# Optimization experiments

Hardware: AMD Instinct MI355X
Metric: run time of the kernel (lower is better)

## Reference

```python
import jax, jax.numpy as jnp
import numpy as np

B, S = 256, 800
N1, N2 = 20000, 60000
NR = N1 + N2
E1, E2 = 60000, 180000
E1G, E2G = 15000, 45000
E1L, E2L = 15000, 45000
NSMT = 600
LAYER_FACTOR = 1e-2
NUM_ACTIVE_LAYERS = 2.0
EPS = 1e-30


def setup_inputs() -> dict:
    key = jax.random.key(0)
    ks = jax.random.split(key, 40)
    u = lambda i, sh: jax.random.uniform(ks[i], sh, jnp.float32)
    ri = lambda i, sh, lo, hi: jax.random.randint(ks[i], sh, lo, hi, dtype=jnp.int32)
    return {
        "t_in": u(0, (B,)),
        "y_in": u(1, (B, S)) * 1e-2,
        "den_gas": 1.0 + 1e4 * u(2, (B, 1)),
        "T_gas": 10.0 + 290.0 * u(3, (B, 1)),
        "alpha": u(4, (NR,)),
        "beta": u(5, (NR,)) * 2.0 - 1.0,
        "gamma": u(6, (NR,)) * 50.0,
        "k1": ri(7, (E1,), 0, N1), "r1": ri(8, (E1,), 0, S), "p1": ri(9, (E1,), 0, S), "s1": ri(10, (E1,), 0, 2),
        "k2": ri(11, (E2,), N1, NR), "ra2": ri(12, (E2,), 0, S), "rb2": ri(13, (E2,), 0, S), "p2": ri(14, (E2,), 0, S), "s2": ri(15, (E2,), 0, 2),
        "k1g": ri(16, (E1G,), 0, N1), "r1g": ri(17, (E1G,), 0, S), "p1g": ri(18, (E1G,), 0, S), "s1g": ri(19, (E1G,), 0, 2),
        "k2g": ri(20, (E2G,), N1, NR), "ra2g": ri(21, (E2G,), 0, S), "rb2g": ri(22, (E2G,), 0, S), "p2g": ri(23, (E2G,), 0, S), "s2g": ri(24, (E2G,), 0, 2),
        "k1l": ri(25, (E1L,), 0, N1), "r1l": ri(26, (E1L,), 0, S), "p1l": ri(27, (E1L,), 0, S), "s1l": ri(28, (E1L,), 0, 2),
        "k2l": ri(29, (E2L,), N1, NR), "ra2l": ri(30, (E2L,), 0, S), "rb2l": ri(31, (E2L,), 0, S), "p2l": ri(32, (E2L,), 0, S), "s2l": ri(33, (E2L,), 0, 2),
        "inds_surf": jnp.arange(200, 500, dtype=jnp.int32),
        "inds_mant": jnp.arange(500, 800, dtype=jnp.int32),
        "inds_smt_s2m": jnp.arange(0, NSMT, dtype=jnp.int32),
        "inds_smt_m2s": jnp.arange(NSMT, 2 * NSMT, dtype=jnp.int32),
    }


def _sgn(s):
    return 2.0 * s.astype(jnp.float32) - 1.0


def _asm1(y, coeffs, k, r, p, s):
    # 1st-order: gather rate coeff + reactant, scatter signed rate into product
    rates = coeffs[:, k] * y[:, r] * _sgn(s)  # [B, E]
    return jnp.zeros((y.shape[0], S), y.dtype).at[:, p].add(rates)


def _asm2(y, coeffs, den, k, ra, rb, p, s):
    # 2nd-order: coeff * y_a * y_b * den_gas, scatter into product
    rates = coeffs[:, k] * y[:, ra] * y[:, rb] * den * _sgn(s)  # [B, E]
    return jnp.zeros((y.shape[0], S), y.dtype).at[:, p].add(rates)


def _forward(t_in, y_in, den_gas, T_gas, alpha, beta, gamma,
             k1, r1, p1, s1, k2, ra2, rb2, p2, s2,
             k1g, r1g, p1g, s1g, k2g, ra2g, rb2g, p2g, s2g,
             k1l, r1l, p1l, s1l, k2l, ra2l, rb2l, p2l, s2l,
             inds_surf, inds_mant, inds_smt_s2m, inds_smt_m2s):
    den = den_gas  # [B,1] density normalization for 2nd-order reactions
    T = T_gas      # [B,1]
    # modified-Arrhenius rate coefficients (rmod.assign_rate_coeffs), [B, NR]
    coeffs = alpha * (T / 300.0) ** beta * jnp.exp(-gamma / T)
    y_surf = y_in[:, inds_surf].sum(-1, keepdims=True)
    y_mant = y_in[:, inds_mant].sum(-1, keepdims=True)
    n_layer_surf = LAYER_FACTOR * y_surf
    n_layer_mant = LAYER_FACTOR * y_mant
    decay = jnp.minimum(NUM_ACTIVE_LAYERS / jnp.maximum(n_layer_surf + n_layer_mant, EPS), 1.0)
    # surface gain/loss assemblers, restricted to surface species then summed
    dy_gain = (_asm1(y_in, coeffs, k1g, r1g, p1g, s1g)
               + _asm2(y_in, coeffs, den, k2g, ra2g, rb2g, p2g, s2g))[:, inds_surf]
    dy_surf_gain = dy_gain.sum(-1, keepdims=True)
    dy_loss = (_asm1(y_in, coeffs, k1l, r1l, p1l, s1l)
               + _asm2(y_in, coeffs, den, k2l, ra2l, rb2l, p2l, s2l))[:, inds_surf]
    dy_surf_loss = -dy_loss.sum(-1, keepdims=True)
    # rmod_smt: surface<->mantle swap rate coefficients scatter-set into coeffs
    Bn = y_in.shape[0]
    k_s2m = jnp.broadcast_to(dy_surf_gain / jnp.maximum(y_surf, EPS), (Bn, NSMT))
    k_m2s = jnp.broadcast_to(-dy_surf_loss / jnp.maximum(y_mant, EPS) * decay, (Bn, NSMT))
    coeffs = coeffs.at[:, inds_smt_s2m].set(k_s2m)
    coeffs = coeffs.at[:, inds_smt_m2s].set(k_m2s)
    # final RHS: asm_1st + asm_2nd over all reactions
    return (_asm1(y_in, coeffs, k1, r1, p1, s1)
            + _asm2(y_in, coeffs, den, k2, ra2, rb2, p2, s2))


def reference(t_in, y_in, den_gas, T_gas, alpha, beta, gamma,
              k1, r1, p1, s1, k2, ra2, rb2, p2, s2,
              k1g, r1g, p1g, s1g, k2g, ra2g, rb2g, p2g, s2g,
              k1l, r1l, p1l, s1l, k2l, ra2l, rb2l, p2l, s2l,
              inds_surf, inds_mant, inds_smt_s2m, inds_smt_m2s):
    return _forward(t_in, y_in, den_gas, T_gas, alpha, beta, gamma,
                    k1, r1, p1, s1, k2, ra2, rb2, p2, s2,
                    k1g, r1g, p1g, s1g, k2g, ra2g, rb2g, p2g, s2g,
                    k1l, r1l, p1l, s1l, k2l, ra2l, rb2l, p2l, s2l,
                    inds_surf, inds_mant, inds_smt_s2m, inds_smt_m2s)
```

## Files before the change

### kernel.cpp

```cpp
#include <hip/hip_runtime.h>


constexpr int B_    = 256;
constexpr int S_    = 800;
constexpr int E1_   = 60000;
constexpr int E2_   = 180000;
constexpr int ET_   = E1_ + E2_;
constexpr int EGL_  = 120000;
constexpr int NSMT_ = 600;
constexpr float LOG2E_ = 1.4426950408889634f;
constexpr float EPS_   = 1e-30f;
constexpr int PAD   = 16;
constexpr int CAPP  = 512;
constexpr int CAP_  = 32768;
constexpr int NBGL_ = 1024;
constexpr int NSL_  = 8;
constexpr int NB_T  = 200;
constexpr int NB_P  = (EGL_ + 255) / 256;
constexpr int NB_R  = (ET_ + 255) / 256;
constexpr int IB_ONE = 800, IB_KS = 801, IB_KM = 802, WROWS = 804;

#if defined(__has_builtin)
#if __has_builtin(__builtin_amdgcn_exp2f)
#define FAST_EXP2(x) __builtin_amdgcn_exp2f(x)
#endif
#endif
#ifndef FAST_EXP2
#define FAST_EXP2(x) exp2f(x)
#endif

__global__ __launch_bounds__(256) void prep_kernel(
    const float* __restrict__ y, const float* __restrict__ den_gas,
    float* __restrict__ yT, float* __restrict__ wT,
    const float* __restrict__ alpha, const float* __restrict__ beta,
    const float* __restrict__ gam,
    const int* __restrict__ k1g, const int* __restrict__ r1g,
    const int* __restrict__ p1g, const int* __restrict__ s1g,
    const int* __restrict__ k2g, const int* __restrict__ ra2g,
    const int* __restrict__ rb2g, const int* __restrict__ p2g,
    const int* __restrict__ s2g,
    const int* __restrict__ k1l, const int* __restrict__ r1l,
    const int* __restrict__ p1l, const int* __restrict__ s1l,
    const int* __restrict__ k2l, const int* __restrict__ ra2l,
    const int* __restrict__ rb2l, const int* __restrict__ p2l,
    const int* __restrict__ s2l,
    int* __restrict__ glcnt, float4* __restrict__ glG, float4* __restrict__ glL)
{
    __shared__ float tile[32][33];
    __shared__ int cntW[2][4];
    __shared__ int baseS[2];

    const int blk = blockIdx.x;
    const int tid = threadIdx.x;

    if (blk < NB_T) {
        const int bi = blk;
        const int sb = bi % 25, bb = bi / 25;
        const int tx = tid & 31, ty = tid >> 5;
        const int s0 = sb * 32, b0 = bb * 32;
        #pragma unroll
        for (int j = 0; j < 4; ++j) {
            int bl = ty + 8 * j;
            tile[bl][tx] = y[(b0 + bl) * S_ + s0 + tx];
        }
        __syncthreads();
        const float d = den_gas[b0 + tx];
        #pragma unroll
        for (int j = 0; j < 4; ++j) {
            int sl = ty + 8 * j;
            float v = tile[tx][sl];
            yT[(s0 + sl) * B_ + b0 + tx] = v;
            wT[(s0 + sl) * B_ + b0 + tx] = v * d;
        }
        if (bi == 0) wT[IB_ONE * B_ + tid] = 1.0f;
        return;
    }
    {
        const int lane = tid & 63, wid = tid >> 6;
        const int e = (blk - NB_T) * 256 + tid;

        int kk = 0, ia = 0, ib = 0, pp = -1, ss = 0, gl = 0;
        if (e < EGL_) {
            if (e < 15000)      { int i = e;         kk = k1g[i]; ia = r1g[i];  ib = IB_ONE;  pp = p1g[i]; ss = s1g[i]; gl = 0; }
            else if (e < 60000) { int i = e - 15000; kk = k2g[i]; ia = ra2g[i]; ib = rb2g[i]; pp = p2g[i]; ss = s2g[i]; gl = 0; }
            else if (e < 75000) { int i = e - 60000; kk = k1l[i]; ia = r1l[i];  ib = IB_ONE;  pp = p1l[i]; ss = s1l[i]; gl = 1; }
            else                { int i = e - 75000; kk = k2l[i]; ia = ra2l[i]; ib = rb2l[i]; pp = p2l[i]; ss = s2l[i]; gl = 1; }
        }
        const bool keep = (pp >= 200 && pp < 500);
        const bool kG = keep && (gl == 0);
        const bool kL = keep && (gl == 1);

        const unsigned long long mG = __ballot(kG);
        const unsigned long long mL = __ballot(kL);
        if (lane == 0) { cntW[0][wid] = __popcll(mG); cntW[1][wid] = __popcll(mL); }
        __syncthreads();
        if (tid < 2) {
            int s = 0;
            #pragma unroll
            for (int w = 0; w < 4; ++w) { int v = cntW[tid][w]; cntW[tid][w] = s; s += v; }
            baseS[tid] = s ? atomicAdd(&glcnt[tid], s) : 0;
        }
        __syncthreads();

        if (keep) {
            float a = alpha[kk], b = beta[kk], g = gam[kk];
            float a_s = ss ? a : -a;
            int bits = ia | (ib << 10);
            const unsigned long long lt = (1ull << lane) - 1ull;
            if (kG) {
                int slot = baseS[0] + cntW[0][wid] + __popcll(mG & lt);
                glG[slot] = make_float4(a_s, b, g, __int_as_float(bits));
            } else {
                int slot = baseS[1] + cntW[1][wid] + __popcll(mL & lt);
                glL[slot] = make_float4(a_s, b, g, __int_as_float(bits));
            }
        }
    }
}

__device__ __forceinline__ float edge_term(
    float4 q, int t, const float* __restrict__ yT, const float* __restrict__ wT,
    float lt2, float nivt)
{
    int bu = __builtin_amdgcn_readfirstlane(__float_as_int(q.w));
    int ia = bu & 1023, ib = (bu >> 10) & 1023;
    return q.x * FAST_EXP2(fmaf(q.y, lt2, q.z * nivt))
         * yT[ia * B_ + t] * wT[ib * B_ + t];
}

__global__ __launch_bounds__(256) void work_kernel(
    const float* __restrict__ alpha, const float* __restrict__ beta,
    const float* __restrict__ gam,
    const int* __restrict__ k1, const int* __restrict__ r1,
    const int* __restrict__ p1, const int* __restrict__ s1,
    const int* __restrict__ k2, const int* __restrict__ ra2,
    const int* __restrict__ rb2, const int* __restrict__ p2,
    const int* __restrict__ s2,
    int* __restrict__ rank, float4* __restrict__ bucket,
    const float* __restrict__ T_gas,
    const float* __restrict__ yT, const float* __restrict__ wT,
    const float4* __restrict__ glG, const float4* __restrict__ glL,
    const int* __restrict__ glcnt,
    float* __restrict__ part_sl)
{
    __shared__ float4 tG[CAP_ / NBGL_], tL[CAP_ / NBGL_];
    const int blk = blockIdx.x;
    const int tid = threadIdx.x;

    if (blk < NB_R) {
        int e = blk * 256 + tid;
        if (e >= ET_) return;
        int kk, ia, ib, pp, ss;
        if (e < E1_) {
            kk = k1[e]; ia = r1[e]; pp = p1[e]; ss = s1[e]; ib = IB_ONE;
        } else {
            int i = e - E1_;
            kk = k2[i]; ia = ra2[i]; ib = rb2[i]; pp = p2[i]; ss = s2[i];
        }
        float a = alpha[kk], b = beta[kk], g = gam[kk];
        if (e < E1_ && kk < 2 * NSMT_) {
            ib = (kk < NSMT_) ? IB_KS : IB_KM;
            a = 1.0f; b = 0.0f; g = 0.0f;
        }
        float a_s = ss ? a : -a;
        int bits = ia | (ib << 10);
        int slot = atomicAdd(&rank[pp * PAD], 1);
        bucket[pp * CAPP + slot] = make_float4(a_s, b, g, __int_as_float(bits));
        return;
    }
    {
        const int t = tid, c = blk - NB_R;
        const int nG = glcnt[0], nL = glcnt[1];
        const int cG = (nG + NBGL_ - 1) >> 10;
        const int cL = (nL + NBGL_ - 1) >> 10;
        const int g0 = c * cG, gn = min(nG, g0 + cG) - g0;
        const int l0 = c * cL, ln = min(nL, l0 + cL) - l0;
        for (int i = t; i < gn; i += 256) tG[i] = glG[g0 + i];
        for (int i = t; i < ln; i += 256) tL[i] = glL[l0 + i];
        __syncthreads();

        const float T    = T_gas[t];
        const float lt2  = log2f(T * (1.0f / 300.0f));
        const float nivt = -LOG2E_ / T;

        float gain = 0.f, loss = 0.f;
        #pragma unroll 4
        for (int i = 0; i < gn; ++i) gain += edge_term(tG[i], t, yT, wT, lt2, nivt);
        #pragma unroll 4
        for (int i = 0; i < ln; ++i) loss += edge_term(tL[i], t, yT, wT, lt2, nivt);

        float* sl = part_sl + (c & (NSL_ - 1)) * (2 * B_);
        atomicAdd(&sl[2 * t + 0], gain);
        atomicAdd(&sl[2 * t + 1], loss);
    }
}

__global__ __launch_bounds__(256) void ksm_kernel(
    const float* __restrict__ y, const float* __restrict__ part_sl,
    float* __restrict__ wT)
{
    const int lane = threadIdx.x & 63, wid = threadIdx.x >> 6;
    const int b = blockIdx.x * 4 + wid;
    float vs = 0.f, vm = 0.f;
    #pragma unroll
    for (int j = 0; j < 5; ++j) {
        int i = lane + 64 * j;
        if (i < 300) { vs += y[b * S_ + 200 + i]; vm += y[b * S_ + 500 + i]; }
    }
    #pragma unroll
    for (int o = 32; o > 0; o >>= 1) {
        vs += __shfl_down(vs, o, 64);
        vm += __shfl_down(vm, o, 64);
    }
    if (lane == 0) {
        float gain = 0.f, loss = 0.f;
        #pragma unroll
        for (int s = 0; s < NSL_; ++s) {
            gain += part_sl[s * (2 * B_) + 2 * b + 0];
            loss += part_sl[s * (2 * B_) + 2 * b + 1];
        }
        float nl = 1e-2f * (vs + vm);
        float decay = fminf(2.0f / fmaxf(nl, EPS_), 1.0f);
        wT[IB_KS * B_ + b] = gain / fmaxf(vs, EPS_);
        wT[IB_KM * B_ + b] = loss / fmaxf(vm, EPS_) * decay;
    }
}

__global__ __launch_bounds__(256) void final_kernel(
    const float* __restrict__ T_gas,
    const float* __restrict__ yT, const float* __restrict__ wT,
    const float4* __restrict__ bucket, const int* __restrict__ rank,
    float* __restrict__ outT)
{
    __shared__ float4 tile[CAPP / 2 + 8];
    const int t = threadIdx.x;
    const int p = blockIdx.x >> 1, h = blockIdx.x & 1;
    const int n  = rank[p * PAD];
    const int n0 = n >> 1;
    const int s0 = h ? n0 : 0;
    const int s1 = h ? n  : n0;
    const int cnt = s1 - s0;

    const float4* src = bucket + p * CAPP + s0;
    for (int i = t; i < cnt; i += 256) tile[i] = src[i];
    __syncthreads();

    const float T    = T_gas[t];
    const float lt2  = log2f(T * (1.0f / 300.0f));
    const float nivt = -LOG2E_ / T;

    float acc = 0.f;
    int i = 0;
    #pragma unroll 1
    for (; i + 8 <= cnt; i += 8) {
        float4 q0 = tile[i + 0], q1 = tile[i + 1];
        float4 q2 = tile[i + 2], q3 = tile[i + 3];
        float4 q4 = tile[i + 4], q5 = tile[i + 5];
        float4 q6 = tile[i + 6], q7 = tile[i + 7];
        int b0 = __builtin_amdgcn_readfirstlane(__float_as_int(q0.w));
        int b1 = __builtin_amdgcn_readfirstlane(__float_as_int(q1.w));
        int b2 = __builtin_amdgcn_readfirstlane(__float_as_int(q2.w));
        int b3 = __builtin_amdgcn_readfirstlane(__float_as_int(q3.w));
        int b4 = __builtin_amdgcn_readfirstlane(__float_as_int(q4.w));
        int b5 = __builtin_amdgcn_readfirstlane(__float_as_int(q5.w));
        int b6 = __builtin_amdgcn_readfirstlane(__float_as_int(q6.w));
        int b7 = __builtin_amdgcn_readfirstlane(__float_as_int(q7.w));
        float y0 = yT[(b0 & 1023) * B_ + t], w0 = wT[((b0 >> 10) & 1023) * B_ + t];
        float y1 = yT[(b1 & 1023) * B_ + t], w1 = wT[((b1 >> 10) & 1023) * B_ + t];
        float y2 = yT[(b2 & 1023) * B_ + t], w2 = wT[((b2 >> 10) & 1023) * B_ + t];
        float y3 = yT[(b3 & 1023) * B_ + t], w3 = wT[((b3 >> 10) & 1023) * B_ + t];
        float y4 = yT[(b4 & 1023) * B_ + t], w4 = wT[((b4 >> 10) & 1023) * B_ + t];
        float y5 = yT[(b5 & 1023) * B_ + t], w5 = wT[((b5 >> 10) & 1023) * B_ + t];
        float y6 = yT[(b6 & 1023) * B_ + t], w6 = wT[((b6 >> 10) & 1023) * B_ + t];
        float y7 = yT[(b7 & 1023) * B_ + t], w7 = wT[((b7 >> 10) & 1023) * B_ + t];
        float t0 = q0.x * FAST_EXP2(fmaf(q0.y, lt2, q0.z * nivt)) * y0 * w0;
        float t1 = q1.x * FAST_EXP2(fmaf(q1.y, lt2, q1.z * nivt)) * y1 * w1;
        float t2 = q2.x * FAST_EXP2(fmaf(q2.y, lt2, q2.z * nivt)) * y2 * w2;
        float t3 = q3.x * FAST_EXP2(fmaf(q3.y, lt2, q3.z * nivt)) * y3 * w3;
        float t4 = q4.x * FAST_EXP2(fmaf(q4.y, lt2, q4.z * nivt)) * y4 * w4;
        float t5 = q5.x * FAST_EXP2(fmaf(q5.y, lt2, q5.z * nivt)) * y5 * w5;
        float t6 = q6.x * FAST_EXP2(fmaf(q6.y, lt2, q6.z * nivt)) * y6 * w6;
        float t7 = q7.x * FAST_EXP2(fmaf(q7.y, lt2, q7.z * nivt)) * y7 * w7;
        acc += ((t0 + t1) + (t2 + t3)) + ((t4 + t5) + (t6 + t7));
    }
    for (; i < cnt; ++i) {
        float4 q = tile[i];
        int bu = __builtin_amdgcn_readfirstlane(__float_as_int(q.w));
        float yv = yT[(bu & 1023) * B_ + t], wv = wT[((bu >> 10) & 1023) * B_ + t];
        acc += q.x * FAST_EXP2(fmaf(q.y, lt2, q.z * nivt)) * yv * wv;
    }

    atomicAdd(&outT[p * B_ + t], acc);
}

__global__ __launch_bounds__(256) void transpose_out_kernel(
    const float* __restrict__ outT, float* __restrict__ out)
{
    __shared__ float tile[32][33];
    const int sb = blockIdx.x % 25, bb = blockIdx.x / 25;
    const int tx = threadIdx.x & 31, ty = threadIdx.x >> 5;
    const int s0 = sb * 32, b0 = bb * 32;

    #pragma unroll
    for (int j = 0; j < 4; ++j) {
        int sl = ty + 8 * j;
        tile[sl][tx] = outT[(s0 + sl) * B_ + b0 + tx];
    }
    __syncthreads();
    #pragma unroll
    for (int j = 0; j < 4; ++j) {
        int bl = ty + 8 * j;
        out[(b0 + bl) * S_ + s0 + tx] = tile[tx][bl];
    }
}

extern "C" void kernel_launch(void* const* d_in, const int* in_sizes, int n_in,
                              void* d_out, int out_size, void* d_ws, size_t ws_size,
                              hipStream_t stream) {
    const float* y       = (const float*)d_in[1];
    const float* den_gas = (const float*)d_in[2];
    const float* T_gas   = (const float*)d_in[3];
    const float* alpha   = (const float*)d_in[4];
    const float* beta    = (const float*)d_in[5];
    const float* gam     = (const float*)d_in[6];
    const int* k1  = (const int*)d_in[7];
    const int* r1  = (const int*)d_in[8];
    const int* p1  = (const int*)d_in[9];
    const int* s1  = (const int*)d_in[10];
    const int* k2  = (const int*)d_in[11];
    const int* ra2 = (const int*)d_in[12];
    const int* rb2 = (const int*)d_in[13];
    const int* p2  = (const int*)d_in[14];
    const int* s2  = (const int*)d_in[15];
    const int* k1g  = (const int*)d_in[16];
    const int* r1g  = (const int*)d_in[17];
    const int* p1g  = (const int*)d_in[18];
    const int* s1g  = (const int*)d_in[19];
    const int* k2g  = (const int*)d_in[20];
    const int* ra2g = (const int*)d_in[21];
    const int* rb2g = (const int*)d_in[22];
    const int* p2g  = (const int*)d_in[23];
    const int* s2g  = (const int*)d_in[24];
    const int* k1l  = (const int*)d_in[25];
    const int* r1l  = (const int*)d_in[26];
    const int* p1l  = (const int*)d_in[27];
    const int* s1l  = (const int*)d_in[28];
    const int* k2l  = (const int*)d_in[29];
    const int* ra2l = (const int*)d_in[30];
    const int* rb2l = (const int*)d_in[31];
    const int* p2l  = (const int*)d_in[32];
    const int* s2l  = (const int*)d_in[33];

    char* wsp = (char*)d_ws;
    size_t off = 0;
    float4* bucket = (float4*)(wsp + off); off += (size_t)S_ * CAPP * 16;
    float4* glG    = (float4*)(wsp + off); off += (size_t)CAP_ * 16;
    float4* glL    = (float4*)(wsp + off); off += (size_t)CAP_ * 16;
    float*  yT     = (float*)(wsp + off);  off += (size_t)S_ * B_ * 4;
    float*  wT     = (float*)(wsp + off);  off += (size_t)WROWS * B_ * 4;
    size_t zoff = off;
    float*  outT    = (float*)(wsp + off); off += (size_t)S_ * B_ * 4;
    int*    rank    = (int*)(wsp + off);   off += (size_t)S_ * PAD * 4;
    float*  part_sl = (float*)(wsp + off); off += (size_t)NSL_ * 2 * B_ * 4;
    int*    glcnt   = (int*)(wsp + off);   off += 64;
    size_t zbytes = off - zoff;

    float* out = (float*)d_out;

    hipMemsetAsync(wsp + zoff, 0, zbytes, stream);

    prep_kernel<<<NB_T + NB_P, 256, 0, stream>>>(
        y, den_gas, yT, wT,
        alpha, beta, gam,
        k1g, r1g, p1g, s1g, k2g, ra2g, rb2g, p2g, s2g,
        k1l, r1l, p1l, s1l, k2l, ra2l, rb2l, p2l, s2l,
        glcnt, glG, glL);

    work_kernel<<<NB_R + NBGL_, 256, 0, stream>>>(
        alpha, beta, gam, k1, r1, p1, s1, k2, ra2, rb2, p2, s2,
        rank, bucket,
        T_gas, yT, wT, glG, glL, glcnt, part_sl);

    ksm_kernel<<<64, 256, 0, stream>>>(y, part_sl, wT);

    final_kernel<<<2 * S_, 256, 0, stream>>>(T_gas, yT, wT, bucket, rank, outT);
    transpose_out_kernel<<<200, 256, 0, stream>>>(outT, out);
}
```

Measured before the change: 78.75 us.

## Fuse ksm and output transpose into final kernel, compute surface/mantle sums in prep

Surface and mantle row sums now come from the prep transpose blocks through LDS and global atomics. The swap coefficients are computed per thread inside the final kernel and substituted for the special wT rows. Each product row gets one block that writes the output directly without an atomic, which removes the ksm kernel, the outT buffer and the transpose kernel. The cost is halving the final grid to 800 blocks, adding per-edge selects, and writing output with a strided, uncoalesced pattern.

```diff
diff --git a/kernel.cpp b/kernel.cpp
--- a/kernel.cpp
+++ b/kernel.cpp
@@ -32,6 +32,7 @@
 __global__ __launch_bounds__(256) void prep_kernel(
     const float* __restrict__ y, const float* __restrict__ den_gas,
     float* __restrict__ yT, float* __restrict__ wT,
+    float* __restrict__ vsum, float* __restrict__ msum,
     const float* __restrict__ alpha, const float* __restrict__ beta,
     const float* __restrict__ gam,
     const int* __restrict__ k1g, const int* __restrict__ r1g,
@@ -47,6 +48,7 @@
     int* __restrict__ glcnt, float4* __restrict__ glG, float4* __restrict__ glL)
 {
     __shared__ float tile[32][33];
+    __shared__ float lds_vs[32], lds_vm[32];
     __shared__ int cntW[2][4];
     __shared__ int baseS[2];
 
@@ -58,6 +60,7 @@
         const int sb = bi % 25, bb = bi / 25;
         const int tx = tid & 31, ty = tid >> 5;
         const int s0 = sb * 32, b0 = bb * 32;
+        if (tid < 32) { lds_vs[tid] = 0.0f; lds_vm[tid] = 0.0f; }
         #pragma unroll
         for (int j = 0; j < 4; ++j) {
             int bl = ty + 8 * j;
@@ -65,12 +68,24 @@
         }
         __syncthreads();
         const float d = den_gas[b0 + tx];
+        float vsp = 0.0f, vmp = 0.0f;
         #pragma unroll
         for (int j = 0; j < 4; ++j) {
             int sl = ty + 8 * j;
+            int s  = s0 + sl;
             float v = tile[tx][sl];
             yT[(s0 + sl) * B_ + b0 + tx] = v;
             wT[(s0 + sl) * B_ + b0 + tx] = v * d;
+            if (s >= 200 && s < 500)      vsp += v;
+            else if (s >= 500)            vmp += v;
+        }
+        if (vsp != 0.0f) atomicAdd(&lds_vs[tx], vsp);
+        if (vmp != 0.0f) atomicAdd(&lds_vm[tx], vmp);
+        __syncthreads();
+        if (tid < 32) {
+            float a = lds_vs[tid], m = lds_vm[tid];
+            if (a != 0.0f) atomicAdd(&vsum[b0 + tid], a);
+            if (m != 0.0f) atomicAdd(&msum[b0 + tid], m);
         }
         if (bi == 0) wT[IB_ONE * B_ + tid] = 1.0f;
         return;
@@ -195,59 +210,38 @@
     }
 }
 
-__global__ __launch_bounds__(256) void ksm_kernel(
-    const float* __restrict__ y, const float* __restrict__ part_sl,
-    float* __restrict__ wT)
-{
-    const int lane = threadIdx.x & 63, wid = threadIdx.x >> 6;
-    const int b = blockIdx.x * 4 + wid;
-    float vs = 0.f, vm = 0.f;
-    #pragma unroll
-    for (int j = 0; j < 5; ++j) {
-        int i = lane + 64 * j;
-        if (i < 300) { vs += y[b * S_ + 200 + i]; vm += y[b * S_ + 500 + i]; }
-    }
-    #pragma unroll
-    for (int o = 32; o > 0; o >>= 1) {
-        vs += __shfl_down(vs, o, 64);
-        vm += __shfl_down(vm, o, 64);
-    }
-    if (lane == 0) {
-        float gain = 0.f, loss = 0.f;
-        #pragma unroll
-        for (int s = 0; s < NSL_; ++s) {
-            gain += part_sl[s * (2 * B_) + 2 * b + 0];
-            loss += part_sl[s * (2 * B_) + 2 * b + 1];
-        }
-        float nl = 1e-2f * (vs + vm);
-        float decay = fminf(2.0f / fmaxf(nl, EPS_), 1.0f);
-        wT[IB_KS * B_ + b] = gain / fmaxf(vs, EPS_);
-        wT[IB_KM * B_ + b] = loss / fmaxf(vm, EPS_) * decay;
-    }
-}
-
 __global__ __launch_bounds__(256) void final_kernel(
     const float* __restrict__ T_gas,
     const float* __restrict__ yT, const float* __restrict__ wT,
     const float4* __restrict__ bucket, const int* __restrict__ rank,
-    float* __restrict__ outT)
+    const float* __restrict__ part_sl,
+    const float* __restrict__ vsum, const float* __restrict__ msum,
+    float* __restrict__ out)
 {
-    __shared__ float4 tile[CAPP / 2 + 8];
+    __shared__ float4 tile[CAPP];
     const int t = threadIdx.x;
-    const int p = blockIdx.x >> 1, h = blockIdx.x & 1;
-    const int n  = rank[p * PAD];
-    const int n0 = n >> 1;
-    const int s0 = h ? n0 : 0;
-    const int s1 = h ? n  : n0;
-    const int cnt = s1 - s0;
-
-    const float4* src = bucket + p * CAPP + s0;
+    const int p = blockIdx.x;
+    const int cnt = rank[p * PAD];
+
+    const float4* src = bucket + p * CAPP;
     for (int i = t; i < cnt; i += 256) tile[i] = src[i];
-    __syncthreads();
+
+    float gain = 0.f, loss = 0.f;
+    #pragma unroll
+    for (int s = 0; s < NSL_; ++s) {
+        gain += part_sl[s * (2 * B_) + 2 * t + 0];
+        loss += part_sl[s * (2 * B_) + 2 * t + 1];
+    }
+    const float vs = vsum[t], vm = msum[t];
+    const float nl = 1e-2f * (vs + vm);
+    const float decay = fminf(2.0f / fmaxf(nl, EPS_), 1.0f);
+    const float ks = gain / fmaxf(vs, EPS_);
+    const float km = loss / fmaxf(vm, EPS_) * decay;
 
     const float T    = T_gas[t];
     const float lt2  = log2f(T * (1.0f / 300.0f));
     const float nivt = -LOG2E_ / T;
+    __syncthreads();
 
     float acc = 0.f;
     int i = 0;
@@ -265,14 +259,26 @@
         int b5 = __builtin_amdgcn_readfirstlane(__float_as_int(q5.w));
         int b6 = __builtin_amdgcn_readfirstlane(__float_as_int(q6.w));
         int b7 = __builtin_amdgcn_readfirstlane(__float_as_int(q7.w));
-        float y0 = yT[(b0 & 1023) * B_ + t], w0 = wT[((b0 >> 10) & 1023) * B_ + t];
-        float y1 = yT[(b1 & 1023) * B_ + t], w1 = wT[((b1 >> 10) & 1023) * B_ + t];
-        float y2 = yT[(b2 & 1023) * B_ + t], w2 = wT[((b2 >> 10) & 1023) * B_ + t];
-        float y3 = yT[(b3 & 1023) * B_ + t], w3 = wT[((b3 >> 10) & 1023) * B_ + t];
-        float y4 = yT[(b4 & 1023) * B_ + t], w4 = wT[((b4 >> 10) & 1023) * B_ + t];
-        float y5 = yT[(b5 & 1023) * B_ + t], w5 = wT[((b5 >> 10) & 1023) * B_ + t];
-        float y6 = yT[(b6 & 1023) * B_ + t], w6 = wT[((b6 >> 10) & 1023) * B_ + t];
-        float y7 = yT[(b7 & 1023) * B_ + t], w7 = wT[((b7 >> 10) & 1023) * B_ + t];
+        int i0 = (b0 >> 10) & 1023, i1 = (b1 >> 10) & 1023;
+        int i2 = (b2 >> 10) & 1023, i3 = (b3 >> 10) & 1023;
+        int i4 = (b4 >> 10) & 1023, i5 = (b5 >> 10) & 1023;
+        int i6 = (b6 >> 10) & 1023, i7 = (b7 >> 10) & 1023;
+        float y0 = yT[(b0 & 1023) * B_ + t], w0 = wT[i0 * B_ + t];
+        float y1 = yT[(b1 & 1023) * B_ + t], w1 = wT[i1 * B_ + t];
+        float y2 = yT[(b2 & 1023) * B_ + t], w2 = wT[i2 * B_ + t];
+        float y3 = yT[(b3 & 1023) * B_ + t], w3 = wT[i3 * B_ + t];
+        float y4 = yT[(b4 & 1023) * B_ + t], w4 = wT[i4 * B_ + t];
+        float y5 = yT[(b5 & 1023) * B_ + t], w5 = wT[i5 * B_ + t];
+        float y6 = yT[(b6 & 1023) * B_ + t], w6 = wT[i6 * B_ + t];
+        float y7 = yT[(b7 & 1023) * B_ + t], w7 = wT[i7 * B_ + t];
+        w0 = (i0 == IB_KS) ? ks : ((i0 == IB_KM) ? km : w0);
+        w1 = (i1 == IB_KS) ? ks : ((i1 == IB_KM) ? km : w1);
+        w2 = (i2 == IB_KS) ? ks : ((i2 == IB_KM) ? km : w2);
+        w3 = (i3 == IB_KS) ? ks : ((i3 == IB_KM) ? km : w3);
+        w4 = (i4 == IB_KS) ? ks : ((i4 == IB_KM) ? km : w4);
+        w5 = (i5 == IB_KS) ? ks : ((i5 == IB_KM) ? km : w5);
+        w6 = (i6 == IB_KS) ? ks : ((i6 == IB_KM) ? km : w6);
+        w7 = (i7 == IB_KS) ? ks : ((i7 == IB_KM) ? km : w7);
         float t0 = q0.x * FAST_EXP2(fmaf(q0.y, lt2, q0.z * nivt)) * y0 * w0;
         float t1 = q1.x * FAST_EXP2(fmaf(q1.y, lt2, q1.z * nivt)) * y1 * w1;
         float t2 = q2.x * FAST_EXP2(fmaf(q2.y, lt2, q2.z * nivt)) * y2 * w2;
@@ -286,32 +292,14 @@
     for (; i < cnt; ++i) {
         float4 q = tile[i];
         int bu = __builtin_amdgcn_readfirstlane(__float_as_int(q.w));
-        float yv = yT[(bu & 1023) * B_ + t], wv = wT[((bu >> 10) & 1023) * B_ + t];
+        int ibx = (bu >> 10) & 1023;
+        float yv = yT[(bu & 1023) * B_ + t];
+        float wv = wT[ibx * B_ + t];
+        wv = (ibx == IB_KS) ? ks : ((ibx == IB_KM) ? km : wv);
         acc += q.x * FAST_EXP2(fmaf(q.y, lt2, q.z * nivt)) * yv * wv;
     }
 
-    atomicAdd(&outT[p * B_ + t], acc);
-}
-
-__global__ __launch_bounds__(256) void transpose_out_kernel(
-    const float* __restrict__ outT, float* __restrict__ out)
-{
-    __shared__ float tile[32][33];
-    const int sb = blockIdx.x % 25, bb = blockIdx.x / 25;
-    const int tx = threadIdx.x & 31, ty = threadIdx.x >> 5;
-    const int s0 = sb * 32, b0 = bb * 32;
-
-    #pragma unroll
-    for (int j = 0; j < 4; ++j) {
-        int sl = ty + 8 * j;
-        tile[sl][tx] = outT[(s0 + sl) * B_ + b0 + tx];
-    }
-    __syncthreads();
-    #pragma unroll
-    for (int j = 0; j < 4; ++j) {
-        int bl = ty + 8 * j;
-        out[(b0 + bl) * S_ + s0 + tx] = tile[tx][bl];
-    }
+    out[t * S_ + p] = acc;
 }
 
 extern "C" void kernel_launch(void* const* d_in, const int* in_sizes, int n_in,
@@ -359,9 +347,10 @@
     float*  yT     = (float*)(wsp + off);  off += (size_t)S_ * B_ * 4;
     float*  wT     = (float*)(wsp + off);  off += (size_t)WROWS * B_ * 4;
     size_t zoff = off;
-    float*  outT    = (float*)(wsp + off); off += (size_t)S_ * B_ * 4;
     int*    rank    = (int*)(wsp + off);   off += (size_t)S_ * PAD * 4;
     float*  part_sl = (float*)(wsp + off); off += (size_t)NSL_ * 2 * B_ * 4;
+    float*  vsum    = (float*)(wsp + off); off += (size_t)B_ * 4;
+    float*  msum    = (float*)(wsp + off); off += (size_t)B_ * 4;
     int*    glcnt   = (int*)(wsp + off);   off += 64;
     size_t zbytes = off - zoff;
 
@@ -370,7 +359,7 @@
     hipMemsetAsync(wsp + zoff, 0, zbytes, stream);
 
     prep_kernel<<<NB_T + NB_P, 256, 0, stream>>>(
-        y, den_gas, yT, wT,
+        y, den_gas, yT, wT, vsum, msum,
         alpha, beta, gam,
         k1g, r1g, p1g, s1g, k2g, ra2g, rb2g, p2g, s2g,
         k1l, r1l, p1l, s1l, k2l, ra2l, rb2l, p2l, s2l,
@@ -381,8 +370,6 @@
         rank, bucket,
         T_gas, yT, wT, glG, glL, glcnt, part_sl);
 
-    ksm_kernel<<<64, 256, 0, stream>>>(y, part_sl, wT);
-
-    final_kernel<<<2 * S_, 256, 0, stream>>>(T_gas, yT, wT, bucket, rank, outT);
-    transpose_out_kernel<<<200, 256, 0, stream>>>(outT, out);
-}
+    final_kernel<<<S_, 256, 0, stream>>>(
+        T_gas, yT, wT, bucket, rank, part_sl, vsum, msum, out);
+}
```

Measured after the change: 89.04 us. 1.13x slower.
